# Optimization experiments

Hardware: AMD Instinct MI355X
Metric: run time of the kernel (lower is better)

Reference implementation:

```python
import jax, jax.numpy as jnp
import numpy as np

B, V, S = 128, 64, 40
D, H, VOC = 256, 256, 20000


def setup_inputs() -> dict:
    key = jax.random.key(0)
    ks = jax.random.split(key, 26)
    g = lambda k, shp: (jax.random.normal(k, shp, dtype=jnp.float32) * 0.02)
    inp = {}
    inp['input_seqs'] = jax.random.randint(ks[0], (B, V, S), 0, VOC + 1)
    inp['mask'] = jnp.zeros((B, V), jnp.float32)
    inp['length'] = jax.random.randint(ks[1], (B,), 1, V + 1)
    inp['seq_time_step'] = jax.random.uniform(ks[2], (B, V), dtype=jnp.float32)
    inp['codemask'] = jnp.zeros((B, V, S), jnp.float32)
    inp['label'] = jax.random.randint(ks[3], (B,), 0, 2)
    # embedding table; padding_idx=-1 in torch == row VOC zeroed
    inp['emb'] = g(ks[4], (VOC + 1, D)).at[VOC].set(0.0)
    # LSTM (single layer, batch_first): torch gate order i,f,g,o
    inp['W_ih'] = g(ks[5], (4 * H, D))
    inp['W_hh'] = g(ks[6], (4 * H, H))
    inp['b_ih'] = g(ks[7], (4 * H,))
    inp['b_hh'] = g(ks[8], (4 * H,))
    # attention projections
    inp['Whk'] = g(ks[9], (D, H))
    inp['bhk'] = g(ks[10], (D,))
    inp['W1'] = g(ks[11], (64, 2 * H))
    inp['b1'] = g(ks[12], (64,))
    inp['W2'] = g(ks[13], (2, 64))
    inp['b2'] = g(ks[14], (2,))
    # classifyer MLP: d -> 4d -> 2d -> 2
    inp['C1W'] = g(ks[15], (4 * D, D))
    inp['C1b'] = g(ks[16], (4 * D,))
    inp['C2W'] = g(ks[17], (2 * D, 4 * D))
    inp['C2b'] = g(ks[18], (2 * D,))
    inp['CoW'] = g(ks[19], (2, 2 * D))
    inp['Cob'] = g(ks[20], (2,))
    return inp


def _lstm(x, W_ih, W_hh, b_ih, b_hh):
    # x: [B,T,D] -> hs: [B,T,H]; torch gate order i,f,g,o
    Bsz = x.shape[0]
    Hd = W_hh.shape[1]
    xg = jnp.einsum('btd,gd->btg', x, W_ih) + b_ih + b_hh  # [B,T,4H]

    def step(carry, xg_t):
        h, c = carry
        gates = xg_t + h @ W_hh.T
        i, f, gg, o = jnp.split(gates, 4, axis=-1)
        i = jax.nn.sigmoid(i); f = jax.nn.sigmoid(f)
        gg = jnp.tanh(gg); o = jax.nn.sigmoid(o)
        c = f * c + i * gg
        h = o * jnp.tanh(c)
        return (h, c), h

    z = jnp.zeros((Bsz, Hd), x.dtype)
    _, hs = jax.lax.scan(step, (z, z), jnp.swapaxes(xg, 0, 1))
    return jnp.swapaxes(hs, 0, 1)


def _classify(h, C1W, C1b, C2W, C2b, CoW, Cob):
    h = jax.nn.relu(h @ C1W.T + C1b)
    h = jax.nn.relu(h @ C2W.T + C2b)
    return h @ CoW.T + Cob


def reference(input_seqs, mask, length, seq_time_step, codemask, label,
              emb, W_ih, W_hh, b_ih, b_hh, Whk, bhk, W1, b1, W2, b2,
              C1W, C1b, C2W, C2b, CoW, Cob):
    # before(): embedding gather -> relu -> sum over codes (eval mode, no dropout)
    v = jax.nn.relu(emb[input_seqs]).sum(-2)  # [B,V,D]
    h = _lstm(v, W_ih, W_hh, b_ih, b_hh)       # [B,V,H]

    # vectorized form of the per-timestep attention loop:
    # bar_v[:,0]=v[:,0]; for i>=1: mix of e_k=v[:,0] and w_hk(h[:,i-1])
    e_k = v[:, :1, :]                                   # [B,1,D]
    wh = h @ Whk.T + bhk                                # [B,V,D]
    wh_prev = wh[:, :-1, :]                             # [B,V-1,D] (h at i-1)
    e_b = jnp.broadcast_to(e_k, wh_prev.shape)
    cat = jnp.concatenate([e_b, wh_prev], axis=-1)      # [B,V-1,2D]
    attn = jax.nn.softmax(jnp.tanh(cat @ W1.T + b1) @ W2.T + b2, axis=-1)
    bar_rest = e_b * attn[..., 0:1] + wh_prev * attn[..., 1:2]
    bar_v = jnp.concatenate([v[:, :1, :], bar_rest], axis=1)  # [B,V,D]

    # GAN stand-in (external injected module): identity
    Dec_V, Gen_V = bar_v, bar_v
    gen_h = _lstm(Gen_V, W_ih, W_hh, b_ih, b_hh)

    og = _classify(h, C1W, C1b, C2W, C2b, CoW, Cob)        # [B,V,2]
    fake = _classify(gen_h, C1W, C1b, C2W, C2b, CoW, Cob)  # [B,V,2]
    final_og = og[:, -1, :]
    final_fake = fake[:, -1, :]
    return (final_og, final_fake, Dec_V, Gen_V, seq_time_step, label)
```

## Files before the change

kernel.cpp:

```cpp
#include <hip/hip_runtime.h>

#define DEV __device__ __forceinline__

typedef float f32x4 __attribute__((ext_vector_type(4)));
typedef short s16x8 __attribute__((ext_vector_type(8)));
typedef short s16x4 __attribute__((ext_vector_type(4)));

DEV unsigned short f2bf(float f){
  unsigned int u = __float_as_uint(f);
  u += 0x7fffu + ((u>>16)&1u);
  return (unsigned short)(u>>16);
}
DEV float bf2f(unsigned short h){ return __uint_as_float(((unsigned int)h)<<16); }

#if __has_builtin(__builtin_amdgcn_rcpf)
DEV float frcp_(float x){ return __builtin_amdgcn_rcpf(x); }
#else
DEV float frcp_(float x){ return 1.f/x; }
#endif
#if __has_builtin(__builtin_amdgcn_exp2f)
DEV float fexp2_(float x){ return __builtin_amdgcn_exp2f(x); }
#else
DEV float fexp2_(float x){ return exp2f(x); }
#endif

DEV float tanh_(float x){
  x = fminf(x, 30.f);
  float e = fexp2_(2.8853900817779268f*x);
  return (e-1.f)*frcp_(e+1.f);
}

DEV unsigned char f2e4m3(float x){
  unsigned int u = __float_as_uint(x);
  unsigned int s = (u>>24)&0x80u;
  unsigned int mag = u & 0x7fffffffu;
  if (mag > 0x43E00000u) mag = 0x43E00000u;
  mag += 0x000FFFFFu + ((mag>>20)&1u);
  int e = (int)(mag>>23) - 120;
  unsigned int m = (mag>>20)&7u;
  unsigned int r = (e<=0) ? 0u : (((unsigned)e<<3)|m);
  return (unsigned char)(s|r);
}

DEV f32x4 mfma_bf16(s16x8 a, s16x8 b, f32x4 c){
  return __builtin_amdgcn_mfma_f32_16x16x32_bf16(a,b,c,0,0,0);
}
DEV f32x4 mfma_fp8(long a, long b, f32x4 c){
  return __builtin_amdgcn_mfma_f32_16x16x32_fp8_fp8(a,b,c,0,0,0);
}

DEV void lds_barrier(){
  asm volatile("s_waitcnt lgkmcnt(0)\n\ts_barrier" ::: "memory");
}

DEV unsigned aload_rlx(unsigned* p){
  return __hip_atomic_load(p, __ATOMIC_RELAXED, __HIP_MEMORY_SCOPE_AGENT);
}
DEV void astore_rlx(unsigned* p, unsigned v){
  __hip_atomic_store(p, v, __ATOMIC_RELAXED, __HIP_MEMORY_SCOPE_AGENT);
}
DEV void aadd_rlx(unsigned* p, unsigned v){
  __hip_atomic_fetch_add(p, v, __ATOMIC_RELAXED, __HIP_MEMORY_SCOPE_AGENT);
}
DEV void spin_rlx(unsigned* p, unsigned tgt){
  while (aload_rlx(p) < tgt) __builtin_amdgcn_s_sleep(2);
  asm volatile("" ::: "memory");
}
DEV void block_wait(unsigned* p, unsigned tgt){
  if (threadIdx.x == 0) spin_rlx(p, tgt);
  __syncthreads();
}
DEV s16x4 aload64(const unsigned short* p){
  unsigned long long v = __hip_atomic_load((unsigned long long*)(void*)p,
      __ATOMIC_RELAXED, __HIP_MEMORY_SCOPE_AGENT);
  union { unsigned long long u; s16x4 s; } c; c.u = v; return c.s;
}
DEV void astore64(unsigned short* p, s16x4 v){
  union { s16x4 s; unsigned long long u; } c; c.s = v;
  __hip_atomic_store((unsigned long long*)(void*)p, c.u,
      __ATOMIC_RELAXED, __HIP_MEMORY_SCOPE_AGENT);
}
DEV s16x8 aload128(const unsigned short* p){
  s16x4 a = aload64(p), b = aload64(p+4);
  s16x8 r;
  r[0]=a[0]; r[1]=a[1]; r[2]=a[2]; r[3]=a[3];
  r[4]=b[0]; r[5]=b[1]; r[6]=b[2]; r[7]=b[3];
  return r;
}
DEV float aloadf(const float* p){
  return __hip_atomic_load((float*)(void*)p, __ATOMIC_RELAXED, __HIP_MEMORY_SCOPE_AGENT);
}
DEV void astoref(float* p, float v){
  __hip_atomic_store(p, v, __ATOMIC_RELAXED, __HIP_MEMORY_SCOPE_AGENT);
}
DEV void vm_drain(){ asm volatile("s_waitcnt vmcnt(0)" ::: "memory"); }
DEV void ntf(float* p, float v){ __builtin_nontemporal_store(v, p); }

#define Bx 128
#define Vx 64
#define Sx 40
#define Dx 256
#define Hx 256
#define NVOC 20001

#define OFF_OG   0
#define OFF_FAKE 256
#define OFF_DECV 512
#define OFF_GENV 2097664
#define OFF_STS  4194816
#define OFF_LBL  4203008

#define PW_IH  0
#define PW_HH  262144
#define PW_HK  524288
#define PW_1   589824
#define PC_1   622592
#define PC_2   884736
#define PC_O   1409024
#define P_TOT  1410048

#define HPB 264
#define BFP 272
#define WHP 272

#define FCT(t) ((t)*32)
#define FXG(t) (2048 + (t)*32)
#define FUC    4096
#define FTOT   4224

__global__ void k_cvt_emb(const float* __restrict__ emb, unsigned short* __restrict__ emb16){
  size_t i = (size_t)blockIdx.x*256 + threadIdx.x;
  emb16[i] = f2bf(emb[i]);
}

__global__ void k_pre(const int* __restrict__ seqs, const unsigned short* __restrict__ emb16,
                      unsigned short* __restrict__ v16,
                      float* __restrict__ decv, float* __restrict__ genv,
                      const float* __restrict__ W_ih, const float* __restrict__ Whh,
                      const float* __restrict__ Whk, const float* __restrict__ W1,
                      const float* __restrict__ C1W, const float* __restrict__ C2W,
                      const float* __restrict__ CoW,
                      unsigned short* __restrict__ pool, unsigned char* __restrict__ whh8,
                      const float* __restrict__ sts, const int* __restrict__ label,
                      float* __restrict__ out, unsigned* __restrict__ flags){
  int bx = blockIdx.x, tid = threadIdx.x;
  if (bx < 8192){
    int bt = bx, d = tid;
    const int* sp = seqs + (size_t)bt*Sx;
    float acc = 0.f;
    #pragma unroll 8
    for (int s=0;s<Sx;s++) acc += fmaxf(bf2f(emb16[(size_t)sp[s]*Dx + d]), 0.f);
    size_t o = (size_t)bt*Dx + d;
    v16[o] = f2bf(acc);
    if ((bt & 63) == 0){ decv[o] = acc; genv[o] = acc; }
    return;
  }
  if (bx < 14724){
    int i = (bx-8192)*256 + tid;
    if (i < P_TOT){
      float v;
      if      (i < PW_HH) v = W_ih[i - PW_IH];
      else if (i < PW_HK) v = Whh [i - PW_HH];
      else if (i < PW_1 ) v = Whk [i - PW_HK];
      else if (i < PC_1 ) v = W1  [i - PW_1 ];
      else if (i < PC_2 ) v = C1W [i - PC_1 ];
      else if (i < PC_O ) v = C2W [i - PC_2 ];
      else                v = CoW [i - PC_O ];
      pool[i] = f2bf(v);
    } else if (i < P_TOT + 262144){
      whh8[i - P_TOT] = f2e4m3(16.f*Whh[i - P_TOT]);
    }
    return;
  }
  for (int i=tid;i<FTOT;i+=256) flags[i] = 0u;
  for (int i=tid;i<Bx*Vx;i+=256) out[OFF_STS + i] = sts[i];
  if (tid < Bx) out[OFF_LBL + tid] = (float)label[tid];
}

template<int MODE_A, int MODE_C, int RELU>
__global__ void k_gemm(const unsigned short* __restrict__ A, const unsigned short* __restrict__ Bw,
                       const float* __restrict__ bias1, const float* __restrict__ bias2,
                       unsigned short* __restrict__ C, int K, int Ntot, float scale){
  int tid = threadIdx.x, w = tid>>6, l = tid&63, lm = l&15, q = l>>4;
  int m0 = blockIdx.x*64;
  int n0 = blockIdx.y*256 + w*64;
  f32x4 acc[4][4];
  #pragma unroll
  for (int nt=0;nt<4;nt++){
    int n = n0 + nt*16 + lm;
    float bz = bias1 ? bias1[n] : 0.f;
    if (bias2) bz += bias2[n];
    #pragma unroll
    for (int mt=0;mt<4;mt++) acc[mt][nt] = (f32x4){bz,bz,bz,bz};
  }
  const s16x8* Arow[4];
  #pragma unroll
  for (int mt=0;mt<4;mt++){
    int m = m0 + mt*16 + lm;
    size_t off = (MODE_A==0) ? (size_t)m*K : ((size_t)(m&127)*Vx + (m>>7))*(size_t)K;
    Arow[mt] = (const s16x8*)(A + off);
  }
  int kkn = K/32;
  for (int kk=0; kk<kkn; kk++){
    s16x8 bfr[4];
    #pragma unroll
    for (int nt=0;nt<4;nt++){
      int n = n0 + nt*16 + lm;
      bfr[nt] = *(const s16x8*)(Bw + (size_t)n*K + kk*32 + q*8);
    }
    #pragma unroll
    for (int mt=0;mt<4;mt++){
      s16x8 afr = Arow[mt][kk*4 + q];
      #pragma unroll
      for (int nt=0;nt<4;nt++)
        acc[mt][nt] = mfma_bf16(afr, bfr[nt], acc[mt][nt]);
    }
  }
  #pragma unroll
  for (int mt=0;mt<4;mt++){
    int mbase = m0 + mt*16 + q*4;
    #pragma unroll
    for (int nt=0;nt<4;nt++){
      int n = n0 + nt*16 + lm;
      if (MODE_C==0){
        #pragma unroll
        for (int r=0;r<4;r++){
          float val = scale*acc[mt][nt][r];
          if (RELU) val = fmaxf(val, 0.f);
          C[(size_t)(mbase+r)*Ntot + n] = f2bf(val);
        }
      } else {
        int tt = mbase>>7, bb = mbase&127;
        int gg = bb>>4;
        s16x4 sv;
        #pragma unroll
        for (int r=0;r<4;r++) sv[r] = (short)f2bf(scale*acc[mt][nt][r]);
        *(s16x4*)(C + (((size_t)tt*8 + gg)*1024 + n)*16 + (bb&15)) = sv;
      }
    }
  }
}

DEV void lstm_act(const f32x4* A, float* cst, float* hv){
  const float K1 = 1.4426950408889634f/256.f;
  #pragma unroll
  for (int r=0;r<4;r++){
    float iv = frcp_(1.f + fexp2_(-K1*A[0][r]));
    float fv = frcp_(1.f + fexp2_(-K1*A[1][r]));
    float eg = fexp2_(2.f*K1*A[2][r]);
    float gv = (eg-1.f)*frcp_(eg+1.f);
    float ov = frcp_(1.f + fexp2_(-K1*A[3][r]));
    float cv = fv*cst[r] + iv*gv;
    cst[r] = cv;
    float ec = fexp2_(2.8853900817779268f*fminf(cv,30.f));
    hv[r] = ov*(ec-1.f)*frcp_(ec+1.f);
  }
}

DEV void store_h_fp8(unsigned char* hn, int q, const float* hv){
#if __has_builtin(__builtin_amdgcn_cvt_pk_fp8_f32)
  int p01 = __builtin_amdgcn_cvt_pk_fp8_f32(16.f*hv[0], 16.f*hv[1], 0, false);
  int p23 = __builtin_amdgcn_cvt_pk_fp8_f32(16.f*hv[2], 16.f*hv[3], 0, false);
  hn[(q*4+0)*HPB] = (unsigned char)p01;
  hn[(q*4+1)*HPB] = (unsigned char)(p01>>8);
  hn[(q*4+2)*HPB] = (unsigned char)p23;
  hn[(q*4+3)*HPB] = (unsigned char)(p23>>8);
#else
  #pragma unroll
  for (int r=0;r<4;r++) hn[(q*4+r)*HPB] = f2e4m3(16.f*hv[r]);
#endif
}

template<int IS1>
DEV void scan_body(unsigned char* smem, const unsigned char* __restrict__ W8,
                   const unsigned short* __restrict__ xg, unsigned short* __restrict__ hist,
                   int g, unsigned* __restrict__ flags){
  unsigned char*  hl  = smem;
  unsigned short* h1b = (unsigned short*)(smem + 8448);
  int tid = threadIdx.x;
  int w = tid>>6, l = tid&63, lm = l&15, q = l>>4;
  int j = w*16 + lm;
  for (int i=tid;i<8448;i+=1024) hl[i] = 0;
  long Bf[4][8];
  #pragma unroll
  for (int qq=0;qq<4;qq++){
    int n = qq*256 + j;
    #pragma unroll
    for (int kk=0;kk<8;kk++)
      Bf[qq][kk] = *(const long*)(W8 + (size_t)n*256 + kk*32 + q*8);
  }
  float cst[4] = {0.f,0.f,0.f,0.f};
  const unsigned short* xgb = xg + (size_t)g*16384 + q*4;
  s16x4 xc[4], xn[4];
  if (!IS1) block_wait(&flags[FXG(0)], 1);
  #pragma unroll
  for (int qq=0;qq<4;qq++){
    const unsigned short* p = xgb + (qq*256+j)*16;
    xc[qq] = IS1 ? *(const s16x4*)p : aload64(p);
  }
  __syncthreads();
  const unsigned char* hrd = hl + lm*HPB + q*8;
  #pragma unroll 1
  for (int t=0;t<Vx;t++){
    if (t < Vx-1){
      if (!IS1) block_wait(&flags[FXG(t+1)], 1);
      #pragma unroll
      for (int qq=0;qq<4;qq++){
        const unsigned short* p = xgb + (size_t)(t+1)*131072 + (qq*256+j)*16;
        xn[qq] = IS1 ? *(const s16x4*)p : aload64(p);
      }
    }
    const unsigned char* hb = hrd + (t&1)*4224;
    f32x4 A[4];
    #pragma unroll
    for (int qq=0;qq<4;qq++){
      #pragma unroll
      for (int r=0;r<4;r++) A[qq][r] = bf2f((unsigned short)xc[qq][r]);
    }
    #pragma unroll
    for (int kk=0;kk<8;kk++){
      long af = *(const long*)(hb + kk*32);
      A[0] = mfma_fp8(af, Bf[0][kk], A[0]);
      A[1] = mfma_fp8(af, Bf[1][kk], A[1]);
      A[2] = mfma_fp8(af, Bf[2][kk], A[2]);
      A[3] = mfma_fp8(af, Bf[3][kk], A[3]);
    }
    float hv[4];
    lstm_act(A, cst, hv);
    store_h_fp8(hl + ((t+1)&1)*4224 + j, q, hv);
    if (IS1){
      #pragma unroll
      for (int r=0;r<4;r++) h1b[(q*4+r)*BFP + j] = f2bf(hv[r]);
      lds_barrier();
      {
        int row = tid>>6, c4 = (tid&63)*4;
        s16x4 hx = *(const s16x4*)(h1b + row*BFP + c4);
        astore64(hist + ((size_t)t*Bx + g*16 + row)*Hx + c4, hx);
      }
      vm_drain();
      __syncthreads();
      if (tid == 0) aadd_rlx(&flags[FCT(t)], 1);
    } else {
      if (t == Vx-1){
        #pragma unroll
        for (int r=0;r<4;r++)
          hist[(size_t)(g*16 + q*4 + r)*Hx + j] = f2bf(hv[r]);
      }
      lds_barrier();
    }
    #pragma unroll
    for (int qq=0;qq<4;qq++) xc[qq] = xn[qq];
  }
}

template<int ALDS>
DEV void xg2_tile(const unsigned short* Ab, const unsigned short* __restrict__ pool,
                  const float* __restrict__ b_ih, const float* __restrict__ b_hh,
                  unsigned short* __restrict__ xg2, int tile, int w, int lm, int q){
  int mh = (w&1)*64, nb = (w>>1)*128;
  #pragma unroll 1
  for (int sc=0; sc<4; sc++){
    int n0 = nb + sc*32;
    f32x4 acc[4][2];
    #pragma unroll
    for (int nt=0;nt<2;nt++){
      int n = n0 + nt*16 + lm;
      float bz = b_ih[n] + b_hh[n];
      #pragma unroll
      for (int mt=0;mt<4;mt++) acc[mt][nt] = (f32x4){bz,bz,bz,bz};
    }
    #pragma unroll
    for (int kk=0;kk<8;kk++){
      s16x8 bfr[2];
      #pragma unroll
      for (int nt=0;nt<2;nt++){
        int n = n0 + nt*16 + lm;
        bfr[nt] = *(const s16x8*)(pool + PW_IH + (size_t)n*256 + kk*32 + q*8);
      }
      #pragma unroll
      for (int mt=0;mt<4;mt++){
        int row = mh + mt*16 + lm;
        s16x8 afr = ALDS ? *(const s16x8*)(Ab + (size_t)row*WHP + kk*32 + q*8)
                         : *(const s16x8*)(Ab + (size_t)row*Vx*Dx + kk*32 + q*8);
        acc[mt][0] = mfma_bf16(afr, bfr[0], acc[mt][0]);
        acc[mt][1] = mfma_bf16(afr, bfr[1], acc[mt][1]);
      }
    }
    #pragma unroll
    for (int mt=0;mt<4;mt++){
      int m = mh + mt*16 + q*4;
      int gg = m>>4;
      #pragma unroll
      for (int nt=0;nt<2;nt++){
        int n = n0 + nt*16 + lm;
        s16x4 sv;
        #pragma unroll
        for (int r=0;r<4;r++) sv[r] = (short)f2bf(256.f*acc[mt][nt][r]);
        astore64(xg2 + (((size_t)tile*8 + gg)*1024 + n)*16 + (m&15), sv);
      }
    }
  }
}

DEV void worker_body(unsigned short* whs, int t,
    const unsigned short* __restrict__ hist1, const unsigned short* __restrict__ v16,
    const float* __restrict__ u, const unsigned short* __restrict__ pool,
    const float* __restrict__ bhk, const float* __restrict__ W2, const float* __restrict__ b2,
    const float* __restrict__ b_ih, const float* __restrict__ b_hh,
    float* __restrict__ decv, float* __restrict__ genv,
    unsigned short* __restrict__ xg2, unsigned* __restrict__ flags){
  int tid = threadIdx.x, w = tid>>6, l = tid&63, lm = l&15, q = l>>4;
  if (t == 63){
    xg2_tile<0>(v16, pool, b_ih, b_hh, xg2, 0, w, lm, q);
    vm_drain();
    __syncthreads();
    if (tid == 0) astore_rlx(&flags[FXG(0)], 1);
    return;
  }
  block_wait(&flags[FCT(t)], 8);
  {
    int r0 = (w&7)*16, n0 = (w>>3)*128;
    const unsigned short* Ar = hist1 + ((size_t)t*Bx + r0 + lm)*Hx;
    f32x4 acc[8];
    #pragma unroll
    for (int nt=0;nt<8;nt++){
      float bz = bhk[n0 + nt*16 + lm];
      acc[nt] = (f32x4){bz,bz,bz,bz};
    }
    #pragma unroll
    for (int kk=0;kk<8;kk++){
      s16x8 afr = aload128(Ar + kk*32 + q*8);
      #pragma unroll
      for (int nt=0;nt<8;nt++){
        int n = n0 + nt*16 + lm;
        s16x8 bfr = *(const s16x8*)(pool + PW_HK + (size_t)n*256 + kk*32 + q*8);
        acc[nt] = mfma_bf16(afr, bfr, acc[nt]);
      }
    }
    #pragma unroll
    for (int nt=0;nt<8;nt++){
      int n = n0 + nt*16 + lm, mb = r0 + q*4;
      #pragma unroll
      for (int r=0;r<4;r++) whs[(size_t)(mb+r)*WHP + n] = f2bf(acc[nt][r]);
    }
  }
  if (tid == 0) spin_rlx(&flags[FUC], 8);
  __syncthreads();
  if (w < 8){
    int m0l = w*16;
    f32x4 a2[4];
    #pragma unroll
    for (int nt=0;nt<4;nt++){
      int n = nt*16 + lm;
      #pragma unroll
      for (int r=0;r<4;r++) a2[nt][r] = aloadf(u + (size_t)(m0l + q*4 + r)*64 + n);
    }
    #pragma unroll
    for (int kk=0;kk<8;kk++){
      s16x8 afr = *(const s16x8*)(whs + (size_t)(m0l+lm)*WHP + kk*32 + q*8);
      #pragma unroll
      for (int nt=0;nt<4;nt++){
        int n = nt*16 + lm;
        s16x8 bfr = *(const s16x8*)(pool + PW_1 + (size_t)n*512 + 256 + kk*32 + q*8);
        a2[nt] = mfma_bf16(afr, bfr, a2[nt]);
      }
    }
    float p0a[4] = {0,0,0,0}, p1a[4] = {0,0,0,0};
    #pragma unroll
    for (int nt=0;nt<4;nt++){
      int n = nt*16 + lm;
      float w2a = W2[n], w2b = W2[64+n];
      #pragma unroll
      for (int r=0;r<4;r++){
        float z = tanh_(a2[nt][r]);
        p0a[r] += z*w2a; p1a[r] += z*w2b;
      }
    }
    #pragma unroll
    for (int s=1;s<16;s<<=1){
      #pragma unroll
      for (int r=0;r<4;r++){ p0a[r] += __shfl_xor(p0a[r], s, 16); p1a[r] += __shfl_xor(p1a[r], s, 16); }
    }
    float bb0 = b2[0], bb1 = b2[1];
    int d0 = lm*16;
    #pragma unroll
    for (int r=0;r<4;r++){
      int b = m0l + q*4 + r;
      float g0 = p0a[r]+bb0, g1 = p1a[r]+bb1;
      float al0 = frcp_(1.f + fexp2_(1.4426950408889634f*(g1-g0)));
      float al1 = 1.f - al0;
      const unsigned short* ek = v16 + (size_t)b*Vx*Dx + d0;
      unsigned short* whp = whs + (size_t)b*WHP + d0;
      size_t ob = ((size_t)b*Vx + (t+1))*Dx + d0;
      #pragma unroll
      for (int c=0;c<2;c++){
        s16x8 e8 = *(const s16x8*)(ek + c*8);
        s16x8 w8 = *(const s16x8*)(whp + c*8);
        s16x8 o16;
        #pragma unroll
        for (int jj=0;jj<8;jj++){
          float o = al0*bf2f((unsigned short)e8[jj]) + al1*bf2f((unsigned short)w8[jj]);
          ntf(decv + ob + c*8 + jj, o);
          ntf(genv + ob + c*8 + jj, o);
          o16[jj] = (short)f2bf(o);
        }
        *(s16x8*)(whp + c*8) = o16;
      }
    }
  }
  __syncthreads();
  xg2_tile<1>(whs, pool, b_ih, b_hh, xg2, t+1, w, lm, q);
  vm_drain();
  __syncthreads();
  if (tid == 0) astore_rlx(&flags[FXG(t+1)], 1);
}

__global__ __launch_bounds__(1024) void k_mega(
    const unsigned char* __restrict__ W8,
    const unsigned short* __restrict__ xg1, unsigned short* __restrict__ xg2,
    unsigned short* __restrict__ hist1, unsigned short* __restrict__ h2,
    const unsigned short* __restrict__ v16, float* __restrict__ u,
    const unsigned short* __restrict__ pool,
    const float* __restrict__ bhk, const float* __restrict__ W2, const float* __restrict__ b2,
    const float* __restrict__ b1, const float* __restrict__ b_ih, const float* __restrict__ b_hh,
    float* __restrict__ decv, float* __restrict__ genv,
    unsigned* __restrict__ flags){
  __shared__ __align__(16) unsigned char smem[69632];
  int blk = blockIdx.x;
  if (blk < 8){
    scan_body<1>(smem, W8, xg1, hist1, blk, flags);
  } else if (blk < 16){
    scan_body<0>(smem, W8, xg2, h2, blk-8, flags);
  } else if (blk < 80){
    worker_body((unsigned short*)smem, blk-16, hist1, v16, u, pool, bhk, W2, b2,
                b_ih, b_hh, decv, genv, xg2, flags);
  } else {
    int t2 = (blk-80)*1024 + threadIdx.x;
    int b = t2>>6, n = t2&63;
    const s16x8* vr = (const s16x8*)(v16 + (size_t)b*Vx*Dx);
    const s16x8* wr = (const s16x8*)(pool + PW_1 + (size_t)n*512);
    float a = b1[n];
    for (int kk=0;kk<32;kk++){
      s16x8 x = vr[kk], ww = wr[kk];
      #pragma unroll
      for (int jj=0;jj<8;jj++) a += bf2f((unsigned short)x[jj])*bf2f((unsigned short)ww[jj]);
    }
    astoref(u + t2, a);
    vm_drain();
    __syncthreads();
    if (threadIdx.x == 0) aadd_rlx(&flags[FUC], 1);
  }
}

__global__ void k_out(const unsigned short* __restrict__ y2, const unsigned short* __restrict__ CoW16,
                      const float* __restrict__ Cob, float* __restrict__ out){
  int tid = blockIdx.x*256 + threadIdx.x;
  int m = tid>>1, n = tid&1;
  const s16x8* yr = (const s16x8*)(y2 + (size_t)m*512);
  const s16x8* wr = (const s16x8*)(CoW16 + (size_t)n*512);
  float a = Cob[n];
  for (int kk=0;kk<64;kk++){
    s16x8 yv = yr[kk], ww = wr[kk];
    #pragma unroll
    for (int jj=0;jj<8;jj++) a += bf2f((unsigned short)yv[jj])*bf2f((unsigned short)ww[jj]);
  }
  int base = (m < 128) ? (OFF_OG + m*2) : (OFF_FAKE + (m-128)*2);
  out[base + n] = a;
}

extern "C" void kernel_launch(void* const* d_in, const int* in_sizes, int n_in,
                              void* d_out, int out_size, void* d_ws, size_t ws_size,
                              hipStream_t stream) {
  const int*   seqs  = (const int*)d_in[0];
  const float* sts   = (const float*)d_in[3];
  const int*   label = (const int*)d_in[5];
  const float* emb   = (const float*)d_in[6];
  const float* W_ih  = (const float*)d_in[7];
  const float* W_hh  = (const float*)d_in[8];
  const float* b_ih  = (const float*)d_in[9];
  const float* b_hh  = (const float*)d_in[10];
  const float* Whk   = (const float*)d_in[11];
  const float* bhk   = (const float*)d_in[12];
  const float* W1    = (const float*)d_in[13];
  const float* b1    = (const float*)d_in[14];
  const float* W2    = (const float*)d_in[15];
  const float* b2    = (const float*)d_in[16];
  const float* C1b   = (const float*)d_in[18];
  const float* C2b   = (const float*)d_in[20];
  const float* Cob   = (const float*)d_in[22];
  float* out = (float*)d_out;

  char* ws = (char*)d_ws;
  unsigned short* v16    = (unsigned short*)(ws + 0);
  unsigned short* xg1    = (unsigned short*)(ws + (4<<20));
  unsigned short* hist1  = (unsigned short*)(ws + (20<<20));
  unsigned short* xg2    = (unsigned short*)(ws + (25<<20));
  unsigned short* emb16  = xg2;
  float*          u      = (float*)(ws + (41<<20));
  unsigned char*  whh8   = (unsigned char*)(ws + (41<<20) + (64<<10));
  unsigned*       flags  = (unsigned*)(ws + (41<<20) + (384<<10));
  unsigned short* pool   = (unsigned short*)(ws + (42<<20));
  unsigned short* y1     = xg1;
  unsigned short* y2     = xg1 + 262144;

  unsigned short* h2 = hist1 + (size_t)Vx*Bx*Hx;
  unsigned short* X  = hist1 + (size_t)(Vx-1)*Bx*Hx;

  float* decv = out + OFF_DECV;
  float* genv = out + OFF_GENV;

  k_cvt_emb<<<dim3(NVOC), dim3(256), 0, stream>>>(emb, emb16);
  k_pre<<<dim3(14725), dim3(256), 0, stream>>>(seqs, emb16, v16, decv, genv,
      W_ih, W_hh, Whk, W1, (const float*)d_in[17], (const float*)d_in[19],
      (const float*)d_in[21], pool, whh8, sts, label, out, flags);
  k_gemm<1,1,0><<<dim3(128,4), dim3(256), 0, stream>>>(v16, pool+PW_IH, b_ih, b_hh, xg1, 256, 1024, 256.f);
  k_mega<<<dim3(88), dim3(1024), 0, stream>>>(whh8, xg1, xg2, hist1, h2, v16, u, pool,
      bhk, W2, b2, b1, b_ih, b_hh, decv, genv, flags);
  k_gemm<0,0,1><<<dim3(4,4), dim3(256), 0, stream>>>(X, pool+PC_1, C1b, nullptr, y1, 256, 1024, 1.f);
  k_gemm<0,0,1><<<dim3(4,2), dim3(256), 0, stream>>>(y1, pool+PC_2, C2b, nullptr, y2, 1024, 512, 1.f);
  k_out<<<dim3(2), dim3(256), 0, stream>>>(y2, pool+PC_O, Cob, out);
}
```

Before: 484.8 us.

## Fold xg1 GEMM and classifier MLP into persistent megakernel with flag-driven overlap

Moves the input-projection GEMM for the first LSTM into extra blocks of the persistent megakernel, publishing per-timestep readiness flags so the first scan can start as soon as its timestep inputs exist. The classifier GEMMs and output layer also become flag-gated blocks inside the megakernel, which removes several launches and their serialisation gaps. The second scan now prefetches inputs two steps ahead, and the weight conversion is merged with the embedding conversion into one launch. The cost is more spin-waiting and a larger grid of 242 blocks of 1024 threads. Correctness depends on all blocks being co-resident, or the spins can deadlock.

```diff
diff --git a/kernel.cpp b/kernel.cpp
--- a/kernel.cpp
+++ b/kernel.cpp
@@ -62,12 +62,17 @@
 DEV void aadd_rlx(unsigned* p, unsigned v){
   __hip_atomic_fetch_add(p, v, __ATOMIC_RELAXED, __HIP_MEMORY_SCOPE_AGENT);
 }
+DEV void acq_fence(){ __builtin_amdgcn_fence(__ATOMIC_ACQUIRE, "agent"); }
 DEV void spin_rlx(unsigned* p, unsigned tgt){
   while (aload_rlx(p) < tgt) __builtin_amdgcn_s_sleep(2);
   asm volatile("" ::: "memory");
 }
 DEV void block_wait(unsigned* p, unsigned tgt){
   if (threadIdx.x == 0) spin_rlx(p, tgt);
+  __syncthreads();
+}
+DEV void block_wait_acq(unsigned* p, unsigned tgt){
+  if (threadIdx.x == 0){ spin_rlx(p, tgt); acq_fence(); }
   __syncthreads();
 }
 DEV s16x4 aload64(const unsigned short* p){
@@ -91,6 +96,9 @@
   return __hip_atomic_load((float*)(void*)p, __ATOMIC_RELAXED, __HIP_MEMORY_SCOPE_AGENT);
 }
 DEV void astoref(float* p, float v){
+  __hip_atomic_store(p, v, __ATOMIC_RELAXED, __HIP_MEMORY_SCOPE_AGENT);
+}
+DEV void astore16(unsigned short* p, unsigned short v){
   __hip_atomic_store(p, v, __ATOMIC_RELAXED, __HIP_MEMORY_SCOPE_AGENT);
 }
 DEV void vm_drain(){ asm volatile("s_waitcnt vmcnt(0)" ::: "memory"); }
@@ -123,19 +131,17 @@
 #define BFP 272
 #define WHP 272
 
-#define FCT(t) ((t)*32)
-#define FXG(t) (2048 + (t)*32)
-#define FUC    4096
-#define FTOT   4224
-
-__global__ void k_cvt_emb(const float* __restrict__ emb, unsigned short* __restrict__ emb16){
-  size_t i = (size_t)blockIdx.x*256 + threadIdx.x;
-  emb16[i] = f2bf(emb[i]);
-}
-
-__global__ void k_pre(const int* __restrict__ seqs, const unsigned short* __restrict__ emb16,
-                      unsigned short* __restrict__ v16,
-                      float* __restrict__ decv, float* __restrict__ genv,
+#define FCT(t)  ((t)*32)
+#define FXG(t)  (2048 + (t)*32)
+#define FUC     4096
+#define FXG1(t) (4352 + (t)*32)
+#define XDONE   6528
+#define Y1D     6656
+#define Y2D     6784
+#define XG1A    6912
+#define FTOT    8192
+
+__global__ void k_cvt(const float* __restrict__ emb, unsigned short* __restrict__ emb16,
                       const float* __restrict__ W_ih, const float* __restrict__ Whh,
                       const float* __restrict__ Whk, const float* __restrict__ W1,
                       const float* __restrict__ C1W, const float* __restrict__ C2W,
@@ -144,19 +150,13 @@
                       const float* __restrict__ sts, const int* __restrict__ label,
                       float* __restrict__ out, unsigned* __restrict__ flags){
   int bx = blockIdx.x, tid = threadIdx.x;
-  if (bx < 8192){
-    int bt = bx, d = tid;
-    const int* sp = seqs + (size_t)bt*Sx;
-    float acc = 0.f;
-    #pragma unroll 8
-    for (int s=0;s<Sx;s++) acc += fmaxf(bf2f(emb16[(size_t)sp[s]*Dx + d]), 0.f);
-    size_t o = (size_t)bt*Dx + d;
-    v16[o] = f2bf(acc);
-    if ((bt & 63) == 0){ decv[o] = acc; genv[o] = acc; }
+  if (bx < NVOC){
+    size_t i = (size_t)bx*256 + tid;
+    emb16[i] = f2bf(emb[i]);
     return;
   }
-  if (bx < 14724){
-    int i = (bx-8192)*256 + tid;
+  if (bx < NVOC + 6532){
+    int i = (bx - NVOC)*256 + tid;
     if (i < P_TOT){
       float v;
       if      (i < PW_HH) v = W_ih[i - PW_IH];
@@ -167,7 +167,7 @@
       else if (i < PC_O ) v = C2W [i - PC_2 ];
       else                v = CoW [i - PC_O ];
       pool[i] = f2bf(v);
-    } else if (i < P_TOT + 262144){
+    } else {
       whh8[i - P_TOT] = f2e4m3(16.f*Whh[i - P_TOT]);
     }
     return;
@@ -177,68 +177,17 @@
   if (tid < Bx) out[OFF_LBL + tid] = (float)label[tid];
 }
 
-template<int MODE_A, int MODE_C, int RELU>
-__global__ void k_gemm(const unsigned short* __restrict__ A, const unsigned short* __restrict__ Bw,
-                       const float* __restrict__ bias1, const float* __restrict__ bias2,
-                       unsigned short* __restrict__ C, int K, int Ntot, float scale){
-  int tid = threadIdx.x, w = tid>>6, l = tid&63, lm = l&15, q = l>>4;
-  int m0 = blockIdx.x*64;
-  int n0 = blockIdx.y*256 + w*64;
-  f32x4 acc[4][4];
-  #pragma unroll
-  for (int nt=0;nt<4;nt++){
-    int n = n0 + nt*16 + lm;
-    float bz = bias1 ? bias1[n] : 0.f;
-    if (bias2) bz += bias2[n];
-    #pragma unroll
-    for (int mt=0;mt<4;mt++) acc[mt][nt] = (f32x4){bz,bz,bz,bz};
-  }
-  const s16x8* Arow[4];
-  #pragma unroll
-  for (int mt=0;mt<4;mt++){
-    int m = m0 + mt*16 + lm;
-    size_t off = (MODE_A==0) ? (size_t)m*K : ((size_t)(m&127)*Vx + (m>>7))*(size_t)K;
-    Arow[mt] = (const s16x8*)(A + off);
-  }
-  int kkn = K/32;
-  for (int kk=0; kk<kkn; kk++){
-    s16x8 bfr[4];
-    #pragma unroll
-    for (int nt=0;nt<4;nt++){
-      int n = n0 + nt*16 + lm;
-      bfr[nt] = *(const s16x8*)(Bw + (size_t)n*K + kk*32 + q*8);
-    }
-    #pragma unroll
-    for (int mt=0;mt<4;mt++){
-      s16x8 afr = Arow[mt][kk*4 + q];
-      #pragma unroll
-      for (int nt=0;nt<4;nt++)
-        acc[mt][nt] = mfma_bf16(afr, bfr[nt], acc[mt][nt]);
-    }
-  }
-  #pragma unroll
-  for (int mt=0;mt<4;mt++){
-    int mbase = m0 + mt*16 + q*4;
-    #pragma unroll
-    for (int nt=0;nt<4;nt++){
-      int n = n0 + nt*16 + lm;
-      if (MODE_C==0){
-        #pragma unroll
-        for (int r=0;r<4;r++){
-          float val = scale*acc[mt][nt][r];
-          if (RELU) val = fmaxf(val, 0.f);
-          C[(size_t)(mbase+r)*Ntot + n] = f2bf(val);
-        }
-      } else {
-        int tt = mbase>>7, bb = mbase&127;
-        int gg = bb>>4;
-        s16x4 sv;
-        #pragma unroll
-        for (int r=0;r<4;r++) sv[r] = (short)f2bf(scale*acc[mt][nt][r]);
-        *(s16x4*)(C + (((size_t)tt*8 + gg)*1024 + n)*16 + (bb&15)) = sv;
-      }
-    }
-  }
+__global__ void k_pre2(const int* __restrict__ seqs, const unsigned short* __restrict__ emb16,
+                       unsigned short* __restrict__ v16,
+                       float* __restrict__ decv, float* __restrict__ genv){
+  int bt = blockIdx.x, d = threadIdx.x;
+  const int* sp = seqs + (size_t)bt*Sx;
+  float acc = 0.f;
+  #pragma unroll 8
+  for (int s=0;s<Sx;s++) acc += fmaxf(bf2f(emb16[(size_t)sp[s]*Dx + d]), 0.f);
+  size_t o = (size_t)bt*Dx + d;
+  v16[o] = f2bf(acc);
+  if ((bt & 63) == 0){ decv[o] = acc; genv[o] = acc; }
 }
 
 DEV void lstm_act(const f32x4* A, float* cst, float* hv){
@@ -271,10 +220,9 @@
 #endif
 }
 
-template<int IS1>
-DEV void scan_body(unsigned char* smem, const unsigned char* __restrict__ W8,
-                   const unsigned short* __restrict__ xg, unsigned short* __restrict__ hist,
-                   int g, unsigned* __restrict__ flags){
+DEV void scan1_body(unsigned char* smem, const unsigned char* __restrict__ W8,
+                    const unsigned short* __restrict__ xg1, unsigned short* __restrict__ hist,
+                    int g, unsigned* __restrict__ flags){
   unsigned char*  hl  = smem;
   unsigned short* h1b = (unsigned short*)(smem + 8448);
   int tid = threadIdx.x;
@@ -290,25 +238,31 @@
       Bf[qq][kk] = *(const long*)(W8 + (size_t)n*256 + kk*32 + q*8);
   }
   float cst[4] = {0.f,0.f,0.f,0.f};
-  const unsigned short* xgb = xg + (size_t)g*16384 + q*4;
+  const unsigned short* xgb = xg1 + (size_t)g*16384 + q*4;
   s16x4 xc[4], xn[4];
-  if (!IS1) block_wait(&flags[FXG(0)], 1);
-  #pragma unroll
-  for (int qq=0;qq<4;qq++){
-    const unsigned short* p = xgb + (qq*256+j)*16;
-    xc[qq] = IS1 ? *(const s16x4*)p : aload64(p);
-  }
-  __syncthreads();
+  block_wait(&flags[FXG1(0)], 2);
+  #pragma unroll
+  for (int qq=0;qq<4;qq++) xc[qq] = aload64(xgb + (qq*256+j)*16);
+  int all1 = 0;
   const unsigned char* hrd = hl + lm*HPB + q*8;
   #pragma unroll 1
   for (int t=0;t<Vx;t++){
+    if (t > 0){
+      asm volatile("s_waitcnt vmcnt(0)" ::: "memory");
+      __syncthreads();
+    }
+    if (tid == 0){
+      if (t > 0) aadd_rlx(&flags[FCT(t-1)], 1);
+      if (t < Vx-1 && !all1){
+        spin_rlx(&flags[FXG1(t+1)], 2);
+        all1 = (aload_rlx(&flags[XG1A]) >= 128);
+      }
+    }
+    __syncthreads();
     if (t < Vx-1){
-      if (!IS1) block_wait(&flags[FXG(t+1)], 1);
-      #pragma unroll
-      for (int qq=0;qq<4;qq++){
-        const unsigned short* p = xgb + (size_t)(t+1)*131072 + (qq*256+j)*16;
-        xn[qq] = IS1 ? *(const s16x4*)p : aload64(p);
-      }
+      #pragma unroll
+      for (int qq=0;qq<4;qq++)
+        xn[qq] = aload64(xgb + (size_t)(t+1)*131072 + (qq*256+j)*16);
     }
     const unsigned char* hb = hrd + (t&1)*4224;
     f32x4 A[4];
@@ -328,28 +282,97 @@
     float hv[4];
     lstm_act(A, cst, hv);
     store_h_fp8(hl + ((t+1)&1)*4224 + j, q, hv);
-    if (IS1){
+    #pragma unroll
+    for (int r=0;r<4;r++) h1b[(q*4+r)*BFP + j] = f2bf(hv[r]);
+    lds_barrier();
+    {
+      int row = tid>>6, c4 = (tid&63)*4;
+      s16x4 hx = *(const s16x4*)(h1b + row*BFP + c4);
+      astore64(hist + ((size_t)t*Bx + g*16 + row)*Hx + c4, hx);
+    }
+    #pragma unroll
+    for (int qq=0;qq<4;qq++) xc[qq] = xn[qq];
+  }
+  asm volatile("s_waitcnt vmcnt(0)" ::: "memory");
+  __syncthreads();
+  if (tid == 0){ aadd_rlx(&flags[FCT(63)], 1); aadd_rlx(&flags[XDONE], 1); }
+}
+
+DEV void scan2_body(unsigned char* smem, const unsigned char* __restrict__ W8,
+                    const unsigned short* __restrict__ xg2, unsigned short* __restrict__ h2,
+                    int g, unsigned* __restrict__ flags){
+  unsigned char*  hl  = smem;
+  unsigned short* h1b = (unsigned short*)(smem + 8448);
+  int tid = threadIdx.x;
+  int w = tid>>6, l = tid&63, lm = l&15, q = l>>4;
+  int j = w*16 + lm;
+  for (int i=tid;i<8448;i+=1024) hl[i] = 0;
+  long Bf[4][8];
+  #pragma unroll
+  for (int qq=0;qq<4;qq++){
+    int n = qq*256 + j;
+    #pragma unroll
+    for (int kk=0;kk<8;kk++)
+      Bf[qq][kk] = *(const long*)(W8 + (size_t)n*256 + kk*32 + q*8);
+  }
+  float cst[4] = {0.f,0.f,0.f,0.f};
+  const unsigned short* xgb = xg2 + (size_t)g*16384 + q*4;
+  s16x4 xc[4], xn1[4], xn2[4];
+  block_wait(&flags[FXG(0)], 1);
+  #pragma unroll
+  for (int qq=0;qq<4;qq++) xc[qq] = aload64(xgb + (qq*256+j)*16);
+  block_wait(&flags[FXG(1)], 1);
+  #pragma unroll
+  for (int qq=0;qq<4;qq++) xn1[qq] = aload64(xgb + 131072 + (qq*256+j)*16);
+  int skip = 0;
+  const unsigned char* hrd = hl + lm*HPB + q*8;
+  #pragma unroll 1
+  for (int t=0;t<Vx;t++){
+    if (t+2 < Vx){
+      if (tid == 0){
+        if (!skip) spin_rlx(&flags[FXG(t+2)], 1);
+        skip = (t+3 < Vx) && (aload_rlx(&flags[FXG(t+3)]) >= 1);
+      }
+      __syncthreads();
+      #pragma unroll
+      for (int qq=0;qq<4;qq++)
+        xn2[qq] = aload64(xgb + (size_t)(t+2)*131072 + (qq*256+j)*16);
+    }
+    const unsigned char* hb = hrd + (t&1)*4224;
+    f32x4 A[4];
+    #pragma unroll
+    for (int qq=0;qq<4;qq++){
+      #pragma unroll
+      for (int r=0;r<4;r++) A[qq][r] = bf2f((unsigned short)xc[qq][r]);
+    }
+    #pragma unroll
+    for (int kk=0;kk<8;kk++){
+      long af = *(const long*)(hb + kk*32);
+      A[0] = mfma_fp8(af, Bf[0][kk], A[0]);
+      A[1] = mfma_fp8(af, Bf[1][kk], A[1]);
+      A[2] = mfma_fp8(af, Bf[2][kk], A[2]);
+      A[3] = mfma_fp8(af, Bf[3][kk], A[3]);
+    }
+    float hv[4];
+    lstm_act(A, cst, hv);
+    store_h_fp8(hl + ((t+1)&1)*4224 + j, q, hv);
+    if (t == Vx-1){
       #pragma unroll
       for (int r=0;r<4;r++) h1b[(q*4+r)*BFP + j] = f2bf(hv[r]);
       lds_barrier();
       {
         int row = tid>>6, c4 = (tid&63)*4;
         s16x4 hx = *(const s16x4*)(h1b + row*BFP + c4);
-        astore64(hist + ((size_t)t*Bx + g*16 + row)*Hx + c4, hx);
-      }
-      vm_drain();
+        astore64(h2 + (size_t)(g*16 + row)*Hx + c4, hx);
+      }
+      asm volatile("s_waitcnt vmcnt(0)" ::: "memory");
       __syncthreads();
-      if (tid == 0) aadd_rlx(&flags[FCT(t)], 1);
+      if (tid == 0) aadd_rlx(&flags[XDONE], 1);
     } else {
-      if (t == Vx-1){
-        #pragma unroll
-        for (int r=0;r<4;r++)
-          hist[(size_t)(g*16 + q*4 + r)*Hx + j] = f2bf(hv[r]);
-      }
       lds_barrier();
     }
     #pragma unroll
-    for (int qq=0;qq<4;qq++) xc[qq] = xn[qq];
+    for (int qq=0;qq<4;qq++){ xc[qq] = xn1[qq]; xn1[qq] = xn2[qq]; }
   }
 }
 
@@ -515,26 +538,131 @@
   if (tid == 0) astore_rlx(&flags[FXG(t+1)], 1);
 }
 
+DEV void xg1_body(const unsigned short* __restrict__ v16, const unsigned short* __restrict__ pool,
+                  const float* __restrict__ b_ih, const float* __restrict__ b_hh,
+                  unsigned short* __restrict__ xg1, int blk, unsigned* __restrict__ flags){
+  int tid = threadIdx.x, w = tid>>6, l = tid&63, lm = l&15, q = l>>4;
+  int m0 = blk*64;
+  int n0 = w*64;
+  f32x4 acc[4][4];
+  #pragma unroll
+  for (int nt=0;nt<4;nt++){
+    int n = n0 + nt*16 + lm;
+    float bz = b_ih[n] + b_hh[n];
+    #pragma unroll
+    for (int mt=0;mt<4;mt++) acc[mt][nt] = (f32x4){bz,bz,bz,bz};
+  }
+  const s16x8* Arow[4];
+  #pragma unroll
+  for (int mt=0;mt<4;mt++){
+    int m = m0 + mt*16 + lm;
+    Arow[mt] = (const s16x8*)(v16 + ((size_t)(m&127)*Vx + (m>>7))*(size_t)Dx);
+  }
+  for (int kk=0; kk<8; kk++){
+    s16x8 bfr[4];
+    #pragma unroll
+    for (int nt=0;nt<4;nt++){
+      int n = n0 + nt*16 + lm;
+      bfr[nt] = *(const s16x8*)(pool + PW_IH + (size_t)n*256 + kk*32 + q*8);
+    }
+    #pragma unroll
+    for (int mt=0;mt<4;mt++){
+      s16x8 afr = Arow[mt][kk*4 + q];
+      #pragma unroll
+      for (int nt=0;nt<4;nt++)
+        acc[mt][nt] = mfma_bf16(afr, bfr[nt], acc[mt][nt]);
+    }
+  }
+  #pragma unroll
+  for (int mt=0;mt<4;mt++){
+    int mbase = m0 + mt*16 + q*4;
+    int tt = mbase>>7, bb = mbase&127;
+    int gg = bb>>4;
+    #pragma unroll
+    for (int nt=0;nt<4;nt++){
+      int n = n0 + nt*16 + lm;
+      s16x4 sv;
+      #pragma unroll
+      for (int r=0;r<4;r++) sv[r] = (short)f2bf(256.f*acc[mt][nt][r]);
+      astore64(xg1 + (((size_t)tt*8 + gg)*1024 + n)*16 + (bb&15), sv);
+    }
+  }
+  vm_drain();
+  __syncthreads();
+  if (tid == 0){ aadd_rlx(&flags[FXG1(blk>>1)], 1); aadd_rlx(&flags[XG1A], 1); }
+}
+
+DEV void cls_gemm(const unsigned short* __restrict__ A, const unsigned short* __restrict__ Bw,
+                  const float* __restrict__ bias, unsigned short* __restrict__ C,
+                  int K, int Ntot, int bxx, int byy){
+  int tid = threadIdx.x, w = tid>>6, l = tid&63, lm = l&15, q = l>>4;
+  int m0 = bxx*64, n0 = byy*256 + w*64;
+  f32x4 acc[4][4];
+  #pragma unroll
+  for (int nt=0;nt<4;nt++){
+    int n = n0 + nt*16 + lm;
+    float bz = bias[n];
+    #pragma unroll
+    for (int mt=0;mt<4;mt++) acc[mt][nt] = (f32x4){bz,bz,bz,bz};
+  }
+  const s16x8* Arow[4];
+  #pragma unroll
+  for (int mt=0;mt<4;mt++)
+    Arow[mt] = (const s16x8*)(A + (size_t)(m0 + mt*16 + lm)*K);
+  int kkn = K/32;
+  for (int kk=0; kk<kkn; kk++){
+    s16x8 bfr[4];
+    #pragma unroll
+    for (int nt=0;nt<4;nt++){
+      int n = n0 + nt*16 + lm;
+      bfr[nt] = *(const s16x8*)(Bw + (size_t)n*K + kk*32 + q*8);
+    }
+    #pragma unroll
+    for (int mt=0;mt<4;mt++){
+      s16x8 afr = Arow[mt][kk*4 + q];
+      #pragma unroll
+      for (int nt=0;nt<4;nt++)
+        acc[mt][nt] = mfma_bf16(afr, bfr[nt], acc[mt][nt]);
+    }
+  }
+  #pragma unroll
+  for (int mt=0;mt<4;mt++){
+    int mbase = m0 + mt*16 + q*4;
+    #pragma unroll
+    for (int nt=0;nt<4;nt++){
+      int n = n0 + nt*16 + lm;
+      #pragma unroll
+      for (int r=0;r<4;r++)
+        astore16(C + (size_t)(mbase+r)*Ntot + n, f2bf(fmaxf(acc[mt][nt][r], 0.f)));
+    }
+  }
+}
+
 __global__ __launch_bounds__(1024) void k_mega(
     const unsigned char* __restrict__ W8,
-    const unsigned short* __restrict__ xg1, unsigned short* __restrict__ xg2,
-    unsigned short* __restrict__ hist1, unsigned short* __restrict__ h2,
+    unsigned short* __restrict__ xg1, unsigned short* __restrict__ xg2,
+    unsigned short* __restrict__ hist1,
     const unsigned short* __restrict__ v16, float* __restrict__ u,
     const unsigned short* __restrict__ pool,
     const float* __restrict__ bhk, const float* __restrict__ W2, const float* __restrict__ b2,
     const float* __restrict__ b1, const float* __restrict__ b_ih, const float* __restrict__ b_hh,
-    float* __restrict__ decv, float* __restrict__ genv,
+    const float* __restrict__ C1b, const float* __restrict__ C2b, const float* __restrict__ Cob,
+    float* __restrict__ decv, float* __restrict__ genv, float* __restrict__ out,
     unsigned* __restrict__ flags){
   __shared__ __align__(16) unsigned char smem[69632];
   int blk = blockIdx.x;
+  unsigned short* X  = hist1 + (size_t)(Vx-1)*Bx*Hx;
+  unsigned short* h2 = hist1 + (size_t)Vx*Bx*Hx;
+  unsigned short* y1 = xg1;
+  unsigned short* y2 = xg1 + 262144;
   if (blk < 8){
-    scan_body<1>(smem, W8, xg1, hist1, blk, flags);
+    scan1_body(smem, W8, xg1, hist1, blk, flags);
   } else if (blk < 16){
-    scan_body<0>(smem, W8, xg2, h2, blk-8, flags);
+    scan2_body(smem, W8, xg2, h2, blk-8, flags);
   } else if (blk < 80){
     worker_body((unsigned short*)smem, blk-16, hist1, v16, u, pool, bhk, W2, b2,
                 b_ih, b_hh, decv, genv, xg2, flags);
-  } else {
+  } else if (blk < 88){
     int t2 = (blk-80)*1024 + threadIdx.x;
     int b = t2>>6, n = t2&63;
     const s16x8* vr = (const s16x8*)(v16 + (size_t)b*Vx*Dx);
@@ -549,23 +677,39 @@
     vm_drain();
     __syncthreads();
     if (threadIdx.x == 0) aadd_rlx(&flags[FUC], 1);
-  }
-}
-
-__global__ void k_out(const unsigned short* __restrict__ y2, const unsigned short* __restrict__ CoW16,
-                      const float* __restrict__ Cob, float* __restrict__ out){
-  int tid = blockIdx.x*256 + threadIdx.x;
-  int m = tid>>1, n = tid&1;
-  const s16x8* yr = (const s16x8*)(y2 + (size_t)m*512);
-  const s16x8* wr = (const s16x8*)(CoW16 + (size_t)n*512);
-  float a = Cob[n];
-  for (int kk=0;kk<64;kk++){
-    s16x8 yv = yr[kk], ww = wr[kk];
-    #pragma unroll
-    for (int jj=0;jj<8;jj++) a += bf2f((unsigned short)yv[jj])*bf2f((unsigned short)ww[jj]);
-  }
-  int base = (m < 128) ? (OFF_OG + m*2) : (OFF_FAKE + (m-128)*2);
-  out[base + n] = a;
+  } else if (blk < 216){
+    xg1_body(v16, pool, b_ih, b_hh, xg1, blk-88, flags);
+  } else if (blk < 232){
+    block_wait_acq(&flags[XDONE], 16);
+    int p = blk-216;
+    if (threadIdx.x < 256) cls_gemm(X, pool+PC_1, C1b, y1, 256, 1024, p&3, p>>2);
+    vm_drain();
+    __syncthreads();
+    if (threadIdx.x == 0) aadd_rlx(&flags[Y1D], 1);
+  } else if (blk < 240){
+    block_wait_acq(&flags[Y1D], 16);
+    int p = blk-232;
+    if (threadIdx.x < 256) cls_gemm(y1, pool+PC_2, C2b, y2, 1024, 512, p&3, p>>2);
+    vm_drain();
+    __syncthreads();
+    if (threadIdx.x == 0) aadd_rlx(&flags[Y2D], 1);
+  } else {
+    block_wait_acq(&flags[Y2D], 8);
+    if (threadIdx.x < 256){
+      int t2 = (blk-240)*256 + threadIdx.x;
+      int m = t2>>1, n = t2&1;
+      const s16x8* yr = (const s16x8*)(y2 + (size_t)m*512);
+      const s16x8* wr = (const s16x8*)(pool + PC_O + (size_t)n*512);
+      float a = Cob[n];
+      for (int kk=0;kk<64;kk++){
+        s16x8 yv = yr[kk], ww = wr[kk];
+        #pragma unroll
+        for (int jj=0;jj<8;jj++) a += bf2f((unsigned short)yv[jj])*bf2f((unsigned short)ww[jj]);
+      }
+      int base = (m < 128) ? (OFF_OG + m*2) : (OFF_FAKE + (m-128)*2);
+      out[base + n] = a;
+    }
+  }
 }
 
 extern "C" void kernel_launch(void* const* d_in, const int* in_sizes, int n_in,
@@ -600,23 +744,14 @@
   unsigned char*  whh8   = (unsigned char*)(ws + (41<<20) + (64<<10));
   unsigned*       flags  = (unsigned*)(ws + (41<<20) + (384<<10));
   unsigned short* pool   = (unsigned short*)(ws + (42<<20));
-  unsigned short* y1     = xg1;
-  unsigned short* y2     = xg1 + 262144;
-
-  unsigned short* h2 = hist1 + (size_t)Vx*Bx*Hx;
-  unsigned short* X  = hist1 + (size_t)(Vx-1)*Bx*Hx;
 
   float* decv = out + OFF_DECV;
   float* genv = out + OFF_GENV;
 
-  k_cvt_emb<<<dim3(NVOC), dim3(256), 0, stream>>>(emb, emb16);
-  k_pre<<<dim3(14725), dim3(256), 0, stream>>>(seqs, emb16, v16, decv, genv,
+  k_cvt<<<dim3(NVOC + 6532 + 1), dim3(256), 0, stream>>>(emb, emb16,
       W_ih, W_hh, Whk, W1, (const float*)d_in[17], (const float*)d_in[19],
       (const float*)d_in[21], pool, whh8, sts, label, out, flags);
-  k_gemm<1,1,0><<<dim3(128,4), dim3(256), 0, stream>>>(v16, pool+PW_IH, b_ih, b_hh, xg1, 256, 1024, 256.f);
-  k_mega<<<dim3(88), dim3(1024), 0, stream>>>(whh8, xg1, xg2, hist1, h2, v16, u, pool,
-      bhk, W2, b2, b1, b_ih, b_hh, decv, genv, flags);
-  k_gemm<0,0,1><<<dim3(4,4), dim3(256), 0, stream>>>(X, pool+PC_1, C1b, nullptr, y1, 256, 1024, 1.f);
-  k_gemm<0,0,1><<<dim3(4,2), dim3(256), 0, stream>>>(y1, pool+PC_2, C2b, nullptr, y2, 1024, 512, 1.f);
-  k_out<<<dim3(2), dim3(256), 0, stream>>>(y2, pool+PC_O, Cob, out);
-}
+  k_pre2<<<dim3(8192), dim3(256), 0, stream>>>(seqs, emb16, v16, decv, genv);
+  k_mega<<<dim3(242), dim3(1024), 0, stream>>>(whh8, xg1, xg2, hist1, v16, u, pool,
+      bhk, W2, b2, b1, b_ih, b_hh, C1b, C2b, Cob, decv, genv, out, flags);
+}
```

Result: slower. 508.9 us (+5.0%).
